# Optimization experiments

Hardware: AMD Instinct MI355X
Metric: run time of the kernel (lower is better)

Reference implementation:

```python
import jax, jax.numpy as jnp
import numpy as np
from jax import lax

R, K = 1000, 80                 # proposals per image, foreground classes
IMG_H, IMG_W = 800.0, 1333.0    # image_shape (h, w) used by Boxes.clip
SCORE_THRESH = 0.05
NMS_THRESH = 0.5
TOPK = 100                      # topk_per_image


def setup_inputs() -> dict:
    key = jax.random.key(0)
    k1, k2, k3 = jax.random.split(key, 3)
    # well-formed class-specific boxes: x1y1 + positive wh
    x1y1 = jax.random.uniform(k1, (R, K, 2)) * jnp.array([IMG_W - 60.0, IMG_H - 60.0])
    wh = jax.random.uniform(k2, (R, K, 2)) * 200.0 + 10.0
    boxes = jnp.concatenate([x1y1, x1y1 + wh], axis=-1).reshape(R, K * 4)
    logits = jax.random.normal(k3, (R, K + 1)) * 2.0
    scores = jax.nn.softmax(logits, axis=-1)  # (R, K+1), last col = background
    return {"boxes": boxes, "scores": scores}


def _iou_matrix(b):
    # b: [R, 4] (x1, y1, x2, y2) -> [R, R] pairwise IoU
    x1, y1, x2, y2 = b[:, 0], b[:, 1], b[:, 2], b[:, 3]
    area = jnp.clip(x2 - x1, 0.0) * jnp.clip(y2 - y1, 0.0)
    xx1 = jnp.maximum(x1[:, None], x1[None, :])
    yy1 = jnp.maximum(y1[:, None], y1[None, :])
    xx2 = jnp.minimum(x2[:, None], x2[None, :])
    yy2 = jnp.minimum(y2[:, None], y2[None, :])
    inter = jnp.clip(xx2 - xx1, 0.0) * jnp.clip(yy2 - yy1, 0.0)
    union = area[:, None] + area[None, :] - inter
    return inter / jnp.maximum(union, 1e-9)


def _nms_one_class(boxes_c, scores_c, valid_c):
    # boxes_c: [R,4], scores_c: [R], valid_c: [R] bool (passed score filter)
    masked = jnp.where(valid_c, scores_c, -jnp.inf)
    order = jnp.argsort(-masked)            # descending score
    b = boxes_c[order]
    s = masked[order]
    v = valid_c[order]
    iou = iou_full = _iou_matrix(b)          # [R, R]
    idx = jnp.arange(R)

    def body(i, keep):
        # box i (if still kept & valid) suppresses later boxes with high IoU
        sup = (iou_full[i] > NMS_THRESH) & keep[i] & (idx > i)
        return keep & ~sup

    keep = lax.fori_loop(0, R, body, v)
    return s, keep, order


def reference(boxes, scores):
    # boxes: (R, K*4), scores: (R, K+1)
    bx = boxes.reshape(R, K, 4)
    # Boxes.clip(image_shape=(h, w)): x in [0, w], y in [0, h]
    bx = jnp.stack([
        jnp.clip(bx[..., 0], 0.0, IMG_W),
        jnp.clip(bx[..., 1], 0.0, IMG_H),
        jnp.clip(bx[..., 2], 0.0, IMG_W),
        jnp.clip(bx[..., 3], 0.0, IMG_H),
    ], axis=-1)

    fg = scores[:, :-1]                                  # (R, K) foreground scores
    thres = jnp.minimum(SCORE_THRESH, (fg.mean() + fg.max()) / 2.0)
    valid = fg > thres                                   # filter_mask

    # per-class batched NMS (equivalent to torchvision batched_nms)
    boxes_k = jnp.transpose(bx, (1, 0, 2))               # [K, R, 4]
    s_sorted, keep, order = jax.vmap(_nms_one_class)(boxes_k, fg.T, valid.T)

    flat = jnp.where(keep, s_sorted, -jnp.inf).reshape(-1)   # [K*R]
    topv, topi = lax.top_k(flat, TOPK)                   # keep[:topk], score-sorted
    cls = topi // R
    pos = topi % R
    prop = order[cls, pos]                               # original proposal index (filter_inds[:,0])
    ok = jnp.isfinite(topv)
    okf = ok.astype(boxes.dtype)

    box_out = bx[prop, cls] * okf[:, None]               # pred_boxes  [TOPK, 4]
    sc_out = jnp.where(ok, topv, 0.0)                    # scores      [TOPK]
    full_out = scores[prop] * okf[:, None]               # full_scores [TOPK, K+1]
    cls_out = (cls * ok).astype(boxes.dtype)             # pred_classes as float col

    # packed result: [boxes(4) | score(1) | class(1) | full_scores(K+1)]
    return jnp.concatenate([box_out, sc_out[:, None], cls_out[:, None], full_out], axis=1)
```

## Files before the change

### kernel.cpp

```cpp
#include <hip/hip_runtime.h>
#include <stdint.h>

typedef unsigned long long u64;
typedef unsigned int u32;

#define R_N 1000
#define K_N 80
#define NCOL 81
#define TOPK_N 100
#define OUT_W 87
#define IMG_W_ 1333.0f
#define IMG_H_ 800.0f
#define CSTR 100
#define CSTRP 101
#define NQUAD ((R_N * NCOL) / 4)
#define NMAX 448
#define WMAX 7
#define KM (K_N * CSTR)
#define POISON 0xAAAAAAAAu

__device__ __forceinline__ u32 f32_order(float f) {
    u32 u = __float_as_uint(f);
    return u ^ (((u32)((int)u >> 31)) | 0x80000000u);
}
__device__ __forceinline__ float f32_unorder(u32 o) {
    u32 u = (o & 0x80000000u) ? (o ^ 0x80000000u) : ~o;
    return __uint_as_float(u);
}

__device__ __forceinline__ void grid_barrier(u32* bar, u32 nblk) {
    __syncthreads();
    if (threadIdx.x == 0) {
        __threadfence();
        if (__hip_atomic_load(bar, __ATOMIC_RELAXED, __HIP_MEMORY_SCOPE_AGENT) == POISON)
            atomicCAS(bar, POISON, 0u);
        __hip_atomic_fetch_add(bar, 1u, __ATOMIC_ACQ_REL, __HIP_MEMORY_SCOPE_AGENT);
        while (__hip_atomic_load(bar, __ATOMIC_ACQUIRE, __HIP_MEMORY_SCOPE_AGENT) < nblk)
            __builtin_amdgcn_s_sleep(2);
    }
    __syncthreads();
}

struct P2 {
    float4 bx4[R_N];
    u64 key_s[R_N];
    u64 pool[NMAX * WMAX];
    float area[R_N];
    u64 keep_words[16];
    int s_n;
};
struct P3 {
    u64 keys[K_N * CSTRP];
    int rnk[TOPK_N];
    u64 wx[TOPK_N];
    int wr[TOPK_N];
    int wn;
};
union SMEM { P2 p2; P3 p3; };

__device__ void run_nms(int c, int tid, int lane, int wv, u64 below, float th,
                        const float* sc, P2& p2,
                        const float* __restrict__ boxes, u64* __restrict__ cand) {
    u64* ukey = p2.pool;
    if (wv == 0) {
        int nn = 0;
        for (int r0 = 0; r0 < R_N; r0 += 64) {
            int r = r0 + lane;
            bool pred = (r < R_N) && (sc[r] > th);
            u64 m = __ballot(pred);
            if (pred) {
                int slot = nn + __popcll(m & below);
                ukey[slot] = ((u64)f32_order(sc[r]) << 32) | (u64)(u32)(R_N - 1 - r);
            }
            nn += __popcll(m);
        }
        if (lane == 0) p2.s_n = nn;
    }
    __syncthreads();
    const int n = p2.s_n;

    for (int j = tid; j < n; j += 256) {
        u64 kj = ukey[j];
        int rank = 0;
        for (int k = 0; k < n; ++k) rank += (ukey[k] > kj) ? 1 : 0;
        int r = (R_N - 1) - (int)(kj & 0xFFFFFFFFull);
        float4 b = ((const float4*)boxes)[r * K_N + c];
        float x1 = fminf(fmaxf(b.x, 0.f), IMG_W_);
        float y1 = fminf(fmaxf(b.y, 0.f), IMG_H_);
        float x2 = fminf(fmaxf(b.z, 0.f), IMG_W_);
        float y2 = fminf(fmaxf(b.w, 0.f), IMG_H_);
        p2.key_s[rank] = kj;
        p2.bx4[rank] = make_float4(x1, y1, x2, y2);
        p2.area[rank] = fmaxf(x2 - x1, 0.f) * fmaxf(y2 - y1, 0.f);
    }
    __syncthreads();

    if (n <= NMAX) {
        const int W = (n + 63) >> 6;
        u64* Mrow = p2.pool;
        const int nh = n >> 1;
        for (int t2 = wv; t2 < 2 * W; t2 += 4) {
            int w = t2 >> 1, ih = t2 & 1;
            int i0 = ih ? nh : 0;
            int i1 = ih ? n : nh;
            int j = w * 64 + lane;
            bool jv = j < n;
            float4 bj = jv ? p2.bx4[j] : make_float4(0.f, 0.f, 0.f, 0.f);
            float aj = jv ? p2.area[j] : 0.f;
            for (int i = i0; i < i1; ++i) {
                float4 bi = p2.bx4[i];
                float ai = p2.area[i];
                float xx1 = fmaxf(bi.x, bj.x), yy1 = fmaxf(bi.y, bj.y);
                float xx2 = fminf(bi.z, bj.z), yy2 = fminf(bi.w, bj.w);
                float inter = fmaxf(xx2 - xx1, 0.f) * fmaxf(yy2 - yy1, 0.f);
                bool sup = jv && (j > i) &&
                           (inter / fmaxf(ai + aj - inter, 1e-9f) > 0.5f);
                u64 m = __ballot(sup);
                if (lane == 0) Mrow[i * W + w] = m;
            }
        }
        __syncthreads();

        if (wv == 0) {
            u64 keep_w = 0;
            if (lane < W) {
                int rem = n - lane * 64;
                keep_w = (rem >= 64) ? ~0ull : ((1ull << rem) - 1ull);
            }
            const int lw = (lane < W) ? lane : 0;
            u64 fifo[8];
#pragma unroll
            for (int d = 0; d < 8; ++d) fifo[d] = (d < n) ? Mrow[d * W + lw] : 0ull;
            for (int ib = 0; ib < n; ib += 8) {
#pragma unroll
                for (int d = 0; d < 8; ++d) {
                    int i = ib + d;
                    if (i >= n) break;
                    u64 row = fifo[d];
                    int ip = i + 8;
                    fifo[d] = (ip < n) ? Mrow[ip * W + lw] : 0ull;
                    u64 kw = __shfl(keep_w, i >> 6);
                    if ((kw >> (i & 63)) & 1ull) keep_w &= ~row;
                }
            }
            if (lane < W) p2.keep_words[lane] = keep_w;
            if (lane >= W && lane < 16) p2.keep_words[lane] = 0;
        }
    } else {
        int* keep = (int*)p2.pool;
        for (int j = tid; j < n; j += 256) keep[j] = 1;
        __syncthreads();
        for (int i = 0; i < n - 1; ++i) {
            __syncthreads();
            if (!keep[i]) continue;
            float4 bi = p2.bx4[i];
            float ai = p2.area[i];
            for (int j = i + 1 + tid; j < n; j += 256) {
                if (!keep[j]) continue;
                float xx1 = fmaxf(bi.x, p2.bx4[j].x), yy1 = fmaxf(bi.y, p2.bx4[j].y);
                float xx2 = fminf(bi.z, p2.bx4[j].z), yy2 = fminf(bi.w, p2.bx4[j].w);
                float inter = fmaxf(xx2 - xx1, 0.f) * fmaxf(yy2 - yy1, 0.f);
                if (inter / fmaxf(ai + p2.area[j] - inter, 1e-9f) > 0.5f) keep[j] = 0;
            }
        }
        __syncthreads();
        if (wv == 0) {
            for (int w = 0; w < 16; ++w) {
                int j = w * 64 + lane;
                u64 m = __ballot((j < n) && keep[j]);
                if (lane == 0) p2.keep_words[w] = m;
            }
        }
    }
    __syncthreads();

    if (wv == 0) {
        int kb = 0;
        for (int j0 = 0; j0 < n; j0 += 64) {
            int j = j0 + lane;
            u64 mw = p2.keep_words[j0 >> 6];
            bool kp = (j < n) && ((mw >> lane) & 1ull);
            u64 mm = __ballot(kp);
            int kr = kb + __popcll(mm & below);
            if (kp && kr < CSTR) {
                u64 kj = p2.key_s[j];
                u32 osc = (u32)(kj >> 32);
                int rr = (R_N - 1) - (int)(kj & 0xFFFFFFFFull);
                int flat = c * R_N + j;
                cand[c * CSTR + kr] =
                    ((u64)osc << 27) | ((u64)(u32)(131071 - flat) << 10) | (u64)(u32)rr;
            }
            kb += __popcll(mm);
        }
        if (kb > CSTR) kb = CSTR;
        for (int kz = kb + lane; kz < CSTR; kz += 64) cand[c * CSTR + kz] = 0;
    }
}

__global__ __launch_bounds__(256, 1) void k_nms(const float* __restrict__ boxes,
                                                const float* __restrict__ scores,
                                                float* __restrict__ hdr,
                                                u64* __restrict__ cand) {
    __shared__ P2 p2;
    __shared__ float sc[R_N];
    __shared__ float s_sum[4], s_max[4];

    const int bid = blockIdx.x, tid = threadIdx.x;
    const int lane = tid & 63, wv = tid >> 6;
    const int c = bid;
    const u64 below = (lane == 0) ? 0ull : (~0ull >> (64 - lane));

    for (int r = tid; r < R_N; r += 256) sc[r] = scores[r * NCOL + c];

    {
        float sum = 0.f, mx = -1e30f;
        int q = bid * 256 + tid;
        if (q < NQUAD) {
            float4 v = ((const float4*)scores)[q];
            int m = (q * 4) % NCOL;
            float vv[4] = {v.x, v.y, v.z, v.w};
#pragma unroll
            for (int e = 0; e < 4; ++e) {
                int mm = m + e; if (mm >= NCOL) mm -= NCOL;
                if (mm != K_N) { sum += vv[e]; mx = fmaxf(mx, vv[e]); }
            }
        }
#pragma unroll
        for (int off = 32; off > 0; off >>= 1) {
            sum += __shfl_down(sum, off);
            mx = fmaxf(mx, __shfl_down(mx, off));
        }
        if (lane == 0) { s_sum[wv] = sum; s_max[wv] = mx; }
        __syncthreads();
        if (tid == 0) {
            hdr[2 * bid] = s_sum[0] + s_sum[1] + s_sum[2] + s_sum[3];
            hdr[2 * bid + 1] = fmaxf(fmaxf(s_max[0], s_max[1]), fmaxf(s_max[2], s_max[3]));
        }
    }

    run_nms(c, tid, lane, wv, below, 0.05f, sc, p2, boxes, cand);
}

__global__ __launch_bounds__(256, 1) void k_top(const float* __restrict__ boxes,
                                                const float* __restrict__ scores,
                                                float* __restrict__ hdr,
                                                u32* __restrict__ bars,
                                                u64* __restrict__ cand,
                                                float* __restrict__ outp) {
    __shared__ SMEM sm;
    __shared__ float sc[R_N];
    __shared__ int s_cnt[4], s_kb[2];
    __shared__ float s_thres;

    const int bid = blockIdx.x, tid = threadIdx.x;
    const int lane = tid & 63, wv = tid >> 6;
    const int c = bid;
    const u64 below = (lane == 0) ? 0ull : (~0ull >> (64 - lane));

    {
        const ulonglong2* cp = (const ulonglong2*)cand;
        int cnt = 0;
        for (int t = tid; t < KM / 2; t += 256) {
            ulonglong2 v = cp[t];
            int e0 = 2 * t;
            int cc2 = e0 / CSTR, pos = e0 - cc2 * CSTR;
            sm.p3.keys[cc2 * CSTRP + pos] = v.x;
            sm.p3.keys[cc2 * CSTRP + pos + 1] = v.y;
            cnt += (v.x != 0ull) + (v.y != 0ull);
        }
#pragma unroll
        for (int off = 32; off > 0; off >>= 1) cnt += __shfl_down(cnt, off);
        if (lane == 0) s_cnt[wv] = cnt;
    }

    if (wv == 0) {
        float S = hdr[2 * lane], M = hdr[2 * lane + 1];
        if (lane + 64 < K_N) {
            S += hdr[2 * (lane + 64)];
            M = fmaxf(M, hdr[2 * (lane + 64) + 1]);
        }
#pragma unroll
        for (int off = 32; off > 0; off >>= 1) {
            S += __shfl_down(S, off);
            M = fmaxf(M, __shfl_down(M, off));
        }
        if (lane == 0)
            s_thres = fminf(0.05f, 0.5f * (S / (float)(R_N * K_N) + M));
    }
    __syncthreads();

    if (s_thres != 0.05f) {
        const float th = s_thres;
        for (int r = tid; r < R_N; r += 256) sc[r] = scores[r * NCOL + c];
        __syncthreads();
        run_nms(c, tid, lane, wv, below, th, sc, sm.p2, boxes, cand);
        grid_barrier(&bars[0], K_N);
        {
            const ulonglong2* cp = (const ulonglong2*)cand;
            int cnt = 0;
            for (int t = tid; t < KM / 2; t += 256) {
                ulonglong2 v = cp[t];
                int e0 = 2 * t;
                int cc2 = e0 / CSTR, pos = e0 - cc2 * CSTR;
                sm.p3.keys[cc2 * CSTRP + pos] = v.x;
                sm.p3.keys[cc2 * CSTRP + pos + 1] = v.y;
                cnt += (v.x != 0ull) + (v.y != 0ull);
            }
#pragma unroll
            for (int off = 32; off > 0; off >>= 1) cnt += __shfl_down(cnt, off);
            if (lane == 0) s_cnt[wv] = cnt;
        }
        __syncthreads();
    }

    {
        const int total = s_cnt[0] + s_cnt[1] + s_cnt[2] + s_cnt[3];
        const int target = total < TOPK_N ? total : TOPK_N;

        if (tid < TOPK_N) sm.p3.rnk[tid] = tid;
        if (tid == 0) sm.p3.wn = 0;
        if (wv < 2) {
            int t = wv * 64 + lane;
            bool nz = (t < CSTR) && (sm.p3.keys[c * CSTRP + t] != 0ull);
            u64 m = __ballot(nz);
            if (lane == 0) s_kb[wv] = __popcll(m);
        }
        __syncthreads();
        const int kb = s_kb[0] + s_kb[1];

        const int TASKS = kb * (K_N - 1);
        for (int g = 0; g * 2048 < TASKS; ++g) {
            int lo[8], hi[8], ii[8], base[8];
            u64 xv[8];
            bool act[8];
#pragma unroll
            for (int s = 0; s < 8; ++s) {
                int t = g * 2048 + s * 256 + tid;
                act[s] = t < TASKS;
                int i = 0, cc2 = 0;
                if (act[s]) { i = t % kb; cc2 = t / kb; }
                cc2 += (cc2 >= c);
                ii[s] = i;
                base[s] = cc2 * CSTRP;
                xv[s] = sm.p3.keys[c * CSTRP + i];
                if (xv[s] == 0ull) act[s] = false;
                lo[s] = 0; hi[s] = CSTR;
            }
#pragma unroll
            for (int st = 0; st < 7; ++st) {
#pragma unroll
                for (int s = 0; s < 8; ++s) {
                    int mid = (lo[s] + hi[s]) >> 1;
                    u64 v = sm.p3.keys[base[s] + mid];
                    bool live = lo[s] < hi[s];
                    bool gt = live && (v > xv[s]);
                    lo[s] = gt ? mid + 1 : lo[s];
                    hi[s] = (live && !gt) ? mid : hi[s];
                }
            }
#pragma unroll
            for (int s = 0; s < 8; ++s)
                if (act[s] && lo[s] > 0) atomicAdd(&sm.p3.rnk[ii[s]], lo[s]);
        }
        __syncthreads();

        if (tid < kb) {
            int r = sm.p3.rnk[tid];
            if (r < target) {
                int idx = atomicAdd(&sm.p3.wn, 1);
                sm.p3.wx[idx] = sm.p3.keys[c * CSTRP + tid];
                sm.p3.wr[idx] = r;
            }
        }
        __syncthreads();
        const int wn = sm.p3.wn;

        for (int e = tid; e < wn * OUT_W; e += 256) {
            int w = e / OUT_W, col = e - w * OUT_W;
            u64 x = sm.p3.wx[w];
            int r = sm.p3.wr[w];
            int prop = (int)(x & 0x3FFull);
            float val;
            if (col < 4) {
                float b = boxes[prop * (K_N * 4) + c * 4 + col];
                float lim = (col & 1) ? IMG_H_ : IMG_W_;
                val = fminf(fmaxf(b, 0.f), lim);
            } else if (col == 4) {
                val = f32_unorder((u32)((x >> 27) & 0xFFFFFFFFull));
            } else if (col == 5) {
                val = (float)c;
            } else {
                val = scores[prop * NCOL + (col - 6)];
            }
            outp[r * OUT_W + col] = val;
        }
        for (int row = target + bid; row < TOPK_N; row += K_N) {
            int ob = row * OUT_W;
            for (int e = tid; e < OUT_W; e += 256) outp[ob + e] = 0.f;
        }
    }
}

extern "C" void kernel_launch(void* const* d_in, const int* in_sizes, int n_in,
                              void* d_out, int out_size, void* d_ws, size_t ws_size,
                              hipStream_t stream) {
    const float* boxes = (const float*)d_in[0];
    const float* scores = (const float*)d_in[1];
    float* hdr = (float*)d_ws;
    u32* bars = (u32*)((char*)d_ws + 768);
    u64* cand = (u64*)((char*)d_ws + 1024);

    k_nms<<<dim3(K_N), dim3(256), 0, stream>>>(boxes, scores, hdr, cand);
    k_top<<<dim3(K_N), dim3(256), 0, stream>>>(boxes, scores, hdr, bars, cand, (float*)d_out);
}
```

Measured before the change: 95.11 us.

## Replace full candidate staging in LDS with per-class counts and global binary search

Each NMS block now writes its kept count to a small workspace array. The top-k kernel loads only its own class's candidate keys into shared memory, and sums the per-class counts instead of copying all 8000 candidate keys from every class into LDS. The cross-class binary search for ranks now reads the other classes' keys straight from global memory (L2) rather than LDS. This removes a large staging copy and its barrier, but the search now depends on global-memory latency, which could cost more than the copy it replaces.

```diff
diff --git a/kernel.cpp b/kernel.cpp
--- a/kernel.cpp
+++ b/kernel.cpp
@@ -12,11 +12,9 @@
 #define IMG_W_ 1333.0f
 #define IMG_H_ 800.0f
 #define CSTR 100
-#define CSTRP 101
 #define NQUAD ((R_N * NCOL) / 4)
 #define NMAX 448
 #define WMAX 7
-#define KM (K_N * CSTR)
 #define POISON 0xAAAAAAAAu
 
 __device__ __forceinline__ u32 f32_order(float f) {
@@ -50,7 +48,7 @@
     int s_n;
 };
 struct P3 {
-    u64 keys[K_N * CSTRP];
+    u64 own[CSTR];
     int rnk[TOPK_N];
     u64 wx[TOPK_N];
     int wr[TOPK_N];
@@ -60,7 +58,8 @@
 
 __device__ void run_nms(int c, int tid, int lane, int wv, u64 below, float th,
                         const float* sc, P2& p2,
-                        const float* __restrict__ boxes, u64* __restrict__ cand) {
+                        const float* __restrict__ boxes, u64* __restrict__ cand,
+                        u32* __restrict__ kbs) {
     u64* ukey = p2.pool;
     if (wv == 0) {
         int nn = 0;
@@ -193,6 +192,7 @@
             kb += __popcll(mm);
         }
         if (kb > CSTR) kb = CSTR;
+        if (lane == 0) kbs[c] = (u32)kb;
         for (int kz = kb + lane; kz < CSTR; kz += 64) cand[c * CSTR + kz] = 0;
     }
 }
@@ -200,6 +200,7 @@
 __global__ __launch_bounds__(256, 1) void k_nms(const float* __restrict__ boxes,
                                                 const float* __restrict__ scores,
                                                 float* __restrict__ hdr,
+                                                u32* __restrict__ kbs,
                                                 u64* __restrict__ cand) {
     __shared__ P2 p2;
     __shared__ float sc[R_N];
@@ -238,18 +239,19 @@
         }
     }
 
-    run_nms(c, tid, lane, wv, below, 0.05f, sc, p2, boxes, cand);
+    run_nms(c, tid, lane, wv, below, 0.05f, sc, p2, boxes, cand, kbs);
 }
 
 __global__ __launch_bounds__(256, 1) void k_top(const float* __restrict__ boxes,
                                                 const float* __restrict__ scores,
                                                 float* __restrict__ hdr,
+                                                u32* __restrict__ kbs,
                                                 u32* __restrict__ bars,
                                                 u64* __restrict__ cand,
                                                 float* __restrict__ outp) {
     __shared__ SMEM sm;
     __shared__ float sc[R_N];
-    __shared__ int s_cnt[4], s_kb[2];
+    __shared__ int s_cnt[2];
     __shared__ float s_thres;
 
     const int bid = blockIdx.x, tid = threadIdx.x;
@@ -257,21 +259,8 @@
     const int c = bid;
     const u64 below = (lane == 0) ? 0ull : (~0ull >> (64 - lane));
 
-    {
-        const ulonglong2* cp = (const ulonglong2*)cand;
-        int cnt = 0;
-        for (int t = tid; t < KM / 2; t += 256) {
-            ulonglong2 v = cp[t];
-            int e0 = 2 * t;
-            int cc2 = e0 / CSTR, pos = e0 - cc2 * CSTR;
-            sm.p3.keys[cc2 * CSTRP + pos] = v.x;
-            sm.p3.keys[cc2 * CSTRP + pos + 1] = v.y;
-            cnt += (v.x != 0ull) + (v.y != 0ull);
-        }
-#pragma unroll
-        for (int off = 32; off > 0; off >>= 1) cnt += __shfl_down(cnt, off);
-        if (lane == 0) s_cnt[wv] = cnt;
-    }
+    u64 ownk = (tid < CSTR) ? cand[c * CSTR + tid] : 0ull;
+    u32 kcnt = (tid < K_N) ? kbs[tid] : 0u;
 
     if (wv == 0) {
         float S = hdr[2 * lane], M = hdr[2 * lane + 1];
@@ -293,111 +282,96 @@
         const float th = s_thres;
         for (int r = tid; r < R_N; r += 256) sc[r] = scores[r * NCOL + c];
         __syncthreads();
-        run_nms(c, tid, lane, wv, below, th, sc, sm.p2, boxes, cand);
+        run_nms(c, tid, lane, wv, below, th, sc, sm.p2, boxes, cand, kbs);
         grid_barrier(&bars[0], K_N);
-        {
-            const ulonglong2* cp = (const ulonglong2*)cand;
-            int cnt = 0;
-            for (int t = tid; t < KM / 2; t += 256) {
-                ulonglong2 v = cp[t];
-                int e0 = 2 * t;
-                int cc2 = e0 / CSTR, pos = e0 - cc2 * CSTR;
-                sm.p3.keys[cc2 * CSTRP + pos] = v.x;
-                sm.p3.keys[cc2 * CSTRP + pos + 1] = v.y;
-                cnt += (v.x != 0ull) + (v.y != 0ull);
-            }
-#pragma unroll
-            for (int off = 32; off > 0; off >>= 1) cnt += __shfl_down(cnt, off);
-            if (lane == 0) s_cnt[wv] = cnt;
-        }
-        __syncthreads();
-    }
-
+        ownk = (tid < CSTR) ? cand[c * CSTR + tid] : 0ull;
+        kcnt = (tid < K_N) ? kbs[tid] : 0u;
+        __syncthreads();
+    }
+
+    if (tid < CSTR) sm.p3.own[tid] = ownk;
+    if (tid < TOPK_N) sm.p3.rnk[tid] = tid;
+    if (tid == 0) sm.p3.wn = 0;
     {
-        const int total = s_cnt[0] + s_cnt[1] + s_cnt[2] + s_cnt[3];
-        const int target = total < TOPK_N ? total : TOPK_N;
-
-        if (tid < TOPK_N) sm.p3.rnk[tid] = tid;
-        if (tid == 0) sm.p3.wn = 0;
-        if (wv < 2) {
-            int t = wv * 64 + lane;
-            bool nz = (t < CSTR) && (sm.p3.keys[c * CSTRP + t] != 0ull);
-            u64 m = __ballot(nz);
-            if (lane == 0) s_kb[wv] = __popcll(m);
-        }
-        __syncthreads();
-        const int kb = s_kb[0] + s_kb[1];
-
-        const int TASKS = kb * (K_N - 1);
-        for (int g = 0; g * 2048 < TASKS; ++g) {
-            int lo[8], hi[8], ii[8], base[8];
-            u64 xv[8];
-            bool act[8];
+        int cnt = (int)kcnt;
+#pragma unroll
+        for (int off = 32; off > 0; off >>= 1) cnt += __shfl_down(cnt, off);
+        if (lane == 0 && wv < 2) s_cnt[wv] = cnt;
+    }
+    __syncthreads();
+    const int total = s_cnt[0] + s_cnt[1];
+    const int target = total < TOPK_N ? total : TOPK_N;
+    const int kb = (int)kbs[c];
+
+    const int TASKS = kb * (K_N - 1);
+    for (int g = 0; g * 2048 < TASKS; ++g) {
+        int lo[8], hi[8], ii[8], base[8];
+        u64 xv[8];
+        bool act[8];
+#pragma unroll
+        for (int s = 0; s < 8; ++s) {
+            int t = g * 2048 + s * 256 + tid;
+            act[s] = t < TASKS;
+            int i = 0, cc2 = 0;
+            if (act[s]) { i = t % kb; cc2 = t / kb; }
+            cc2 += (cc2 >= c);
+            ii[s] = i;
+            base[s] = cc2 * CSTR;
+            xv[s] = sm.p3.own[i];
+            if (xv[s] == 0ull) act[s] = false;
+            lo[s] = 0; hi[s] = CSTR;
+        }
+#pragma unroll
+        for (int st = 0; st < 7; ++st) {
 #pragma unroll
             for (int s = 0; s < 8; ++s) {
-                int t = g * 2048 + s * 256 + tid;
-                act[s] = t < TASKS;
-                int i = 0, cc2 = 0;
-                if (act[s]) { i = t % kb; cc2 = t / kb; }
-                cc2 += (cc2 >= c);
-                ii[s] = i;
-                base[s] = cc2 * CSTRP;
-                xv[s] = sm.p3.keys[c * CSTRP + i];
-                if (xv[s] == 0ull) act[s] = false;
-                lo[s] = 0; hi[s] = CSTR;
-            }
-#pragma unroll
-            for (int st = 0; st < 7; ++st) {
-#pragma unroll
-                for (int s = 0; s < 8; ++s) {
-                    int mid = (lo[s] + hi[s]) >> 1;
-                    u64 v = sm.p3.keys[base[s] + mid];
-                    bool live = lo[s] < hi[s];
-                    bool gt = live && (v > xv[s]);
-                    lo[s] = gt ? mid + 1 : lo[s];
-                    hi[s] = (live && !gt) ? mid : hi[s];
-                }
-            }
-#pragma unroll
-            for (int s = 0; s < 8; ++s)
-                if (act[s] && lo[s] > 0) atomicAdd(&sm.p3.rnk[ii[s]], lo[s]);
-        }
-        __syncthreads();
-
-        if (tid < kb) {
-            int r = sm.p3.rnk[tid];
-            if (r < target) {
-                int idx = atomicAdd(&sm.p3.wn, 1);
-                sm.p3.wx[idx] = sm.p3.keys[c * CSTRP + tid];
-                sm.p3.wr[idx] = r;
-            }
-        }
-        __syncthreads();
-        const int wn = sm.p3.wn;
-
-        for (int e = tid; e < wn * OUT_W; e += 256) {
-            int w = e / OUT_W, col = e - w * OUT_W;
-            u64 x = sm.p3.wx[w];
-            int r = sm.p3.wr[w];
-            int prop = (int)(x & 0x3FFull);
-            float val;
-            if (col < 4) {
-                float b = boxes[prop * (K_N * 4) + c * 4 + col];
-                float lim = (col & 1) ? IMG_H_ : IMG_W_;
-                val = fminf(fmaxf(b, 0.f), lim);
-            } else if (col == 4) {
-                val = f32_unorder((u32)((x >> 27) & 0xFFFFFFFFull));
-            } else if (col == 5) {
-                val = (float)c;
-            } else {
-                val = scores[prop * NCOL + (col - 6)];
-            }
-            outp[r * OUT_W + col] = val;
-        }
-        for (int row = target + bid; row < TOPK_N; row += K_N) {
-            int ob = row * OUT_W;
-            for (int e = tid; e < OUT_W; e += 256) outp[ob + e] = 0.f;
-        }
+                int mid = (lo[s] + hi[s]) >> 1;
+                u64 v = cand[base[s] + mid];
+                bool live = lo[s] < hi[s];
+                bool gt = live && (v > xv[s]);
+                lo[s] = gt ? mid + 1 : lo[s];
+                hi[s] = (live && !gt) ? mid : hi[s];
+            }
+        }
+#pragma unroll
+        for (int s = 0; s < 8; ++s)
+            if (act[s] && lo[s] > 0) atomicAdd(&sm.p3.rnk[ii[s]], lo[s]);
+    }
+    __syncthreads();
+
+    if (tid < kb) {
+        int r = sm.p3.rnk[tid];
+        if (r < target) {
+            int idx = atomicAdd(&sm.p3.wn, 1);
+            sm.p3.wx[idx] = sm.p3.own[tid];
+            sm.p3.wr[idx] = r;
+        }
+    }
+    __syncthreads();
+    const int wn = sm.p3.wn;
+
+    for (int e = tid; e < wn * OUT_W; e += 256) {
+        int w = e / OUT_W, col = e - w * OUT_W;
+        u64 x = sm.p3.wx[w];
+        int r = sm.p3.wr[w];
+        int prop = (int)(x & 0x3FFull);
+        float val;
+        if (col < 4) {
+            float b = boxes[prop * (K_N * 4) + c * 4 + col];
+            float lim = (col & 1) ? IMG_H_ : IMG_W_;
+            val = fminf(fmaxf(b, 0.f), lim);
+        } else if (col == 4) {
+            val = f32_unorder((u32)((x >> 27) & 0xFFFFFFFFull));
+        } else if (col == 5) {
+            val = (float)c;
+        } else {
+            val = scores[prop * NCOL + (col - 6)];
+        }
+        outp[r * OUT_W + col] = val;
+    }
+    for (int row = target + bid; row < TOPK_N; row += K_N) {
+        int ob = row * OUT_W;
+        for (int e = tid; e < OUT_W; e += 256) outp[ob + e] = 0.f;
     }
 }
 
@@ -407,9 +381,10 @@
     const float* boxes = (const float*)d_in[0];
     const float* scores = (const float*)d_in[1];
     float* hdr = (float*)d_ws;
-    u32* bars = (u32*)((char*)d_ws + 768);
+    u32* kbs = (u32*)((char*)d_ws + 640);
+    u32* bars = (u32*)((char*)d_ws + 960);
     u64* cand = (u64*)((char*)d_ws + 1024);
 
-    k_nms<<<dim3(K_N), dim3(256), 0, stream>>>(boxes, scores, hdr, cand);
-    k_top<<<dim3(K_N), dim3(256), 0, stream>>>(boxes, scores, hdr, bars, cand, (float*)d_out);
-}
+    k_nms<<<dim3(K_N), dim3(256), 0, stream>>>(boxes, scores, hdr, kbs, cand);
+    k_top<<<dim3(K_N), dim3(256), 0, stream>>>(boxes, scores, hdr, kbs, bars, cand, (float*)d_out);
+}
```

After: 99.79 us. 4.9% more time.
